# Optimization experiments

Measured on AMD Instinct MI355X. Metric: run time of the kernel, lower is better.

The kernel has to match this reference:

```python
import jax, jax.numpy as jnp
import numpy as np

FACTOR = 3.0  # maxval of the per-image std uniform draw


def setup_inputs() -> dict:
    key = jax.random.key(0)
    k1, k2 = jax.random.split(key)
    x = jax.random.uniform(k1, (64, 512, 512, 3), dtype=jnp.float32)
    stds = jax.random.uniform(k2, (64,), dtype=jnp.float32)  # uniform [0,1), scaled by FACTOR in reference
    return {"x": x, "stds": stds}


def reference(x, stds):
    # Faithful port of AddingGaussianBlur. Note the original has ys = tf.cast(xs, ...)
    # (a bug), so the kernel depends only on the column coordinate; we reproduce it.
    B, H, W, C = x.shape
    std = stds * FACTOR  # per-image std ~ Uniform(0, factor), shape [B]
    xs_row = jnp.arange(-1, 2, dtype=jnp.float32)          # [-1, 0, 1]
    xs = jnp.broadcast_to(xs_row[None, :], (3, 3))          # meshgrid xs (rows repeat)
    s = std[:, None, None]                                  # [B,1,1]
    # k = exp(-(xs^2 + ys^2)/(2 std^2)) / (2 pi std^2) with ys == xs
    k = jnp.exp(-(xs**2 + xs**2) / (2.0 * s**2)) / (2.0 * np.pi * s**2)  # [B,3,3]
    k = k / jnp.sum(k, axis=(1, 2), keepdims=True)
    # SAME zero-padded 3x3 cross-correlation, same kernel for all 3 channels,
    # per-sample kernel: expressed as weighted sum of 9 shifted views (fully batched).
    xpad = jnp.pad(x, ((0, 0), (1, 1), (1, 1), (0, 0)))
    out = jnp.zeros_like(x)
    for di in range(3):
        for dj in range(3):
            out = out + k[:, di, dj][:, None, None, None] * xpad[:, di:di + H, dj:dj + W, :]
    return out
```

## Files before the change

kernel.cpp:

```cpp
#include <hip/hip_runtime.h>
#include <math.h>


constexpr int Wd   = 512;
constexpr int Hd   = 512;
constexpr int Cd   = 3;
constexpr int ROWF = Wd * Cd;
constexpr int TPB  = ROWF / 4;

__global__ __launch_bounds__(TPB) void gauss_row_kernel(
    const float* __restrict__ x,
    const float* __restrict__ stds,
    float* __restrict__ out)
{
    __shared__ float4 cs[TPB + 2];

    const int t  = threadIdx.x;
    const int bi = blockIdx.x;
    const int i  = bi & (Hd - 1);
    const int b  = bi >> 9;

    const float s  = stds[b] * 3.0f;
    const float e  = expf(-1.0f / (s * s));
    const float w1 = 1.0f / (3.0f * (1.0f + 2.0f * e));
    const float w0 = e * w1;

    const float* row = x + (size_t)bi * ROWF + (size_t)t * 4;

    float4 m = *(const float4*)(row);
    if (i > 0) {
        float4 a = *(const float4*)(row - ROWF);
        m.x += a.x; m.y += a.y; m.z += a.z; m.w += a.w;
    }
    if (i < Hd - 1) {
        float4 a = *(const float4*)(row + ROWF);
        m.x += a.x; m.y += a.y; m.z += a.z; m.w += a.w;
    }

    if (t == 0) {
        cs[0]       = make_float4(0.f, 0.f, 0.f, 0.f);
        cs[TPB + 1] = make_float4(0.f, 0.f, 0.f, 0.f);
    }
    cs[t + 1] = m;
    __syncthreads();

    const float4 p = cs[t];
    const float4 n = cs[t + 2];

    float4 o;
    o.x = w1 * m.x + w0 * (p.y + m.w);
    o.y = w1 * m.y + w0 * (p.z + n.x);
    o.z = w1 * m.z + w0 * (p.w + n.y);
    o.w = w1 * m.w + w0 * (m.x + n.z);

    ((float4*)(out + (size_t)bi * ROWF))[t] = o;
}

extern "C" void kernel_launch(void* const* d_in, const int* in_sizes, int n_in,
                              void* d_out, int out_size, void* d_ws, size_t ws_size,
                              hipStream_t stream) {
    const float* x    = (const float*)d_in[0];
    const float* stds = (const float*)d_in[1];
    float* out        = (float*)d_out;

    const int nblocks = 64 * Hd;
    gauss_row_kernel<<<nblocks, TPB, 0, stream>>>(x, stds, out);
}
```

Before: 335.5 us.

## Process row strips per block with rolling register window and nontemporal stores

```diff
diff --git a/kernel.cpp b/kernel.cpp
--- a/kernel.cpp
+++ b/kernel.cpp
@@ -2,58 +2,73 @@
 #include <math.h>
 
 
-constexpr int Wd   = 512;
-constexpr int Hd   = 512;
-constexpr int Cd   = 3;
-constexpr int ROWF = Wd * Cd;
-constexpr int TPB  = ROWF / 4;
+constexpr int Wd     = 512;
+constexpr int Hd     = 512;
+constexpr int Cd     = 3;
+constexpr int ROWF   = Wd * Cd;
+constexpr int TPB    = ROWF / 4;
+constexpr int RPB    = 32;
+constexpr int STRIPS = Hd / RPB;
 
-__global__ __launch_bounds__(TPB) void gauss_row_kernel(
+using f4 = __attribute__((ext_vector_type(4))) float;
+
+__device__ __forceinline__ f4 f4zero() { return (f4){0.f, 0.f, 0.f, 0.f}; }
+
+__global__ __launch_bounds__(TPB) void gauss_strip_kernel(
     const float* __restrict__ x,
     const float* __restrict__ stds,
     float* __restrict__ out)
 {
-    __shared__ float4 cs[TPB + 2];
+    __shared__ f4 cs[2][TPB + 2];
 
-    const int t  = threadIdx.x;
-    const int bi = blockIdx.x;
-    const int i  = bi & (Hd - 1);
-    const int b  = bi >> 9;
+    const int t = threadIdx.x;
+    const int s = blockIdx.x % STRIPS;
+    const int b = blockIdx.x / STRIPS;
 
-    const float s  = stds[b] * 3.0f;
-    const float e  = expf(-1.0f / (s * s));
+    const float sg = stds[b] * 3.0f;
+    const float e  = expf(-1.0f / (sg * sg));
     const float w1 = 1.0f / (3.0f * (1.0f + 2.0f * e));
     const float w0 = e * w1;
 
-    const float* row = x + (size_t)bi * ROWF + (size_t)t * 4;
+    const size_t imgbase = (size_t)b * Hd * ROWF;
+    const float* px = x   + imgbase + (size_t)t * 4;
+    float*       po = out + imgbase + (size_t)t * 4;
 
-    float4 m = *(const float4*)(row);
-    if (i > 0) {
-        float4 a = *(const float4*)(row - ROWF);
-        m.x += a.x; m.y += a.y; m.z += a.z; m.w += a.w;
-    }
-    if (i < Hd - 1) {
-        float4 a = *(const float4*)(row + ROWF);
-        m.x += a.x; m.y += a.y; m.z += a.z; m.w += a.w;
+    const int r0 = s * RPB;
+
+    f4 ra = (r0 > 0) ? *(const f4*)(px + (size_t)(r0 - 1) * ROWF) : f4zero();
+    f4 rb = *(const f4*)(px + (size_t)r0 * ROWF);
+    f4 rc = *(const f4*)(px + (size_t)(r0 + 1) * ROWF);
+
+    if (t == 0) {
+        cs[0][0] = cs[0][TPB + 1] = f4zero();
+        cs[1][0] = cs[1][TPB + 1] = f4zero();
     }
 
-    if (t == 0) {
-        cs[0]       = make_float4(0.f, 0.f, 0.f, 0.f);
-        cs[TPB + 1] = make_float4(0.f, 0.f, 0.f, 0.f);
+    #pragma unroll 2
+    for (int j = r0; j < r0 + RPB; ++j) {
+        f4 rn = (j + 2 < Hd) ? *(const f4*)(px + (size_t)(j + 2) * ROWF)
+                             : f4zero();
+
+        f4 m = ra + rb + rc;
+
+        f4* buf = cs[j & 1];
+        buf[t + 1] = m;
+        __syncthreads();
+
+        const f4 p = buf[t];
+        const f4 n = buf[t + 2];
+
+        f4 o;
+        o.x = w1 * m.x + w0 * (p.y + m.w);
+        o.y = w1 * m.y + w0 * (p.z + n.x);
+        o.z = w1 * m.z + w0 * (p.w + n.y);
+        o.w = w1 * m.w + w0 * (m.x + n.z);
+
+        __builtin_nontemporal_store(o, (f4*)(po + (size_t)j * ROWF));
+
+        ra = rb; rb = rc; rc = rn;
     }
-    cs[t + 1] = m;
-    __syncthreads();
-
-    const float4 p = cs[t];
-    const float4 n = cs[t + 2];
-
-    float4 o;
-    o.x = w1 * m.x + w0 * (p.y + m.w);
-    o.y = w1 * m.y + w0 * (p.z + n.x);
-    o.z = w1 * m.z + w0 * (p.w + n.y);
-    o.w = w1 * m.w + w0 * (m.x + n.z);
-
-    ((float4*)(out + (size_t)bi * ROWF))[t] = o;
 }
 
 extern "C" void kernel_launch(void* const* d_in, const int* in_sizes, int n_in,
@@ -63,6 +78,6 @@
     const float* stds = (const float*)d_in[1];
     float* out        = (float*)d_out;
 
-    const int nblocks = 64 * Hd;
-    gauss_row_kernel<<<nblocks, TPB, 0, stream>>>(x, stds, out);
+    const int nblocks = 64 * STRIPS;
+    gauss_strip_kernel<<<nblocks, TPB, 0, stream>>>(x, stds, out);
 }
```

After: 346.6 us. +3.3%, slower.
